# Performance work log

Measured on AMD Instinct MI355X. Metric: run time of the kernel, lower is better.

The kernel has to match this reference:

```python
import jax, jax.numpy as jnp
import numpy as np

IN_FEAT = 512   # input_feature_size
ACT_FEAT = 512  # action_feature_size
HIDDEN = 1024   # output_feature_size
L, B = 128, 64


def setup_inputs() -> dict:
    key = jax.random.key(0)
    ks = jax.random.split(key, 4)
    scale = 1.0 / np.sqrt(HIDDEN)
    return {
        "input_feature": jax.random.normal(ks[0], (B, IN_FEAT), jnp.float32),
        "action_features_data": jax.random.normal(ks[1], (L, B, ACT_FEAT), jnp.float32),
        "hidden_state": jnp.zeros((B, HIDDEN), jnp.float32),
        "state": jnp.zeros((B, HIDDEN), jnp.float32),
        "W_ih": jax.random.normal(ks[2], (4 * HIDDEN, IN_FEAT + ACT_FEAT), jnp.float32) * scale,
        "W_hh": jax.random.normal(ks[3], (4 * HIDDEN, HIDDEN), jnp.float32) * scale,
        "b_ih": jnp.zeros((4 * HIDDEN,), jnp.float32),
        "b_hh": jnp.zeros((4 * HIDDEN,), jnp.float32),
    }


def _lstm_forward(input_feature, acts, h0, c0, W_ih, W_hh, b_ih, b_hh):
    H = h0.shape[-1]
    # Split the input weight into the static (input_feature) and per-step (action) parts.
    W_x = W_ih[:, : input_feature.shape[-1]]   # [4H, in_feat]
    W_a = W_ih[:, input_feature.shape[-1]:]    # [4H, act_feat]
    # Precompute all input-side gate preactivations in one big GEMM: [L, B, 4H]
    pre = jnp.einsum("lba,ga->lbg", acts, W_a) + (input_feature @ W_x.T + b_ih + b_hh)

    def step(carry, pre_t):
        h, c = carry
        gates = pre_t + h @ W_hh.T            # [B, 4H]
        i, f, g, o = jnp.split(gates, 4, axis=-1)  # torch LSTMCell gate order
        i = jax.nn.sigmoid(i)
        f = jax.nn.sigmoid(f)
        g = jnp.tanh(g)
        o = jax.nn.sigmoid(o)
        c1 = f * c + i * g
        h1 = o * jnp.tanh(c1)
        return (h1, c1), h1

    (h_n, c_n), hs = jax.lax.scan(step, (h0, c0), pre)
    return hs, h_n, c_n


def reference(input_feature, action_features_data, hidden_state, state,
              W_ih, W_hh, b_ih, b_hh):
    return _lstm_forward(input_feature, action_features_data, hidden_state, state,
                         W_ih, W_hh, b_ih, b_hh)
```

## Files before the change

kernel.cpp:

```cpp
#include <hip/hip_runtime.h>
#include <hip/hip_bf16.h>

typedef __bf16 bf16x8 __attribute__((ext_vector_type(8)));
typedef float f32x4 __attribute__((ext_vector_type(4)));
typedef unsigned long long ull;

#define HN_OFF 8388608u
#define CN_OFF 8454144u

__device__ __forceinline__ float bf2f(ushort u) {
  union { unsigned int i; float f; } x; x.i = ((unsigned int)u) << 16; return x.f;
}
__device__ __forceinline__ ushort f2bf(float f) {
  union { float f; unsigned int i; } x; x.f = f;
  unsigned int r = x.i + 0x7FFFu + ((x.i >> 16) & 1u);
  return (ushort)(r >> 16);
}

__global__ __launch_bounds__(256) void conv_copy(const float* __restrict__ s,
                                                 ushort* __restrict__ d, int n4) {
  int i = blockIdx.x * 256 + threadIdx.x;
  if (i < n4) {
    float4 v = reinterpret_cast<const float4*>(s)[i];
    ushort4 o; o.x = f2bf(v.x); o.y = f2bf(v.y); o.z = f2bf(v.z); o.w = f2bf(v.w);
    reinterpret_cast<ushort4*>(d)[i] = o;
  }
}

__global__ __launch_bounds__(256) void conv_h0(const float* __restrict__ h0,
                                               ushort* __restrict__ hb) {
  int t = blockIdx.x * 256 + threadIdx.x;
  int b = t >> 7, c = t & 127;
  float4 v0 = *reinterpret_cast<const float4*>(h0 + (size_t)b * 1024 + c * 8);
  float4 v1 = *reinterpret_cast<const float4*>(h0 + (size_t)b * 1024 + c * 8 + 4);
  size_t de = ((size_t)(b >> 4) * 32 + (c >> 2)) * 512 + (size_t)(c & 3) * 128 + (b & 15) * 8;
  ushort* d = hb + de;
  d[0] = f2bf(v0.x); d[1] = f2bf(v0.y); d[2] = f2bf(v0.z); d[3] = f2bf(v0.w);
  d[4] = f2bf(v1.x); d[5] = f2bf(v1.y); d[6] = f2bf(v1.z); d[7] = f2bf(v1.w);
}

__global__ __launch_bounds__(256) void conv_wa(const float* __restrict__ Wih,
                                               ushort* __restrict__ Wa) {
  int t = blockIdx.x * 256 + threadIdx.x;
  int g = t >> 7, c = t & 127;
  float4 v = *reinterpret_cast<const float4*>(Wih + (size_t)g * 1024 + 512 + c * 4);
  ushort4 o; o.x = f2bf(v.x); o.y = f2bf(v.y); o.z = f2bf(v.z); o.w = f2bf(v.w);
  *reinterpret_cast<ushort4*>(Wa + (size_t)g * 512 + c * 4) = o;
}

__global__ __launch_bounds__(256) void base_kernel(const float* __restrict__ x,
    const float* __restrict__ Wih, const float* __restrict__ bih,
    const float* __restrict__ bhh, float* __restrict__ baseT) {
  int t = blockIdx.x * 256 + threadIdx.x;
  int g = t >> 6, b = t & 63;
  const float4* xv = reinterpret_cast<const float4*>(x + (size_t)b * 512);
  const float4* wv = reinterpret_cast<const float4*>(Wih + (size_t)g * 1024);
  float s = 0.f;
  #pragma unroll 4
  for (int a = 0; a < 128; ++a) {
    float4 xa = xv[a], wa = wv[a];
    s += xa.x * wa.x + xa.y * wa.y + xa.z * wa.z + xa.w * wa.w;
  }
  baseT[t] = s + bih[g] + bhh[g];
}

__global__ __launch_bounds__(256, 1) void gemm_pre(
    const ushort* __restrict__ A,
    const ushort* __restrict__ B,
    const float* __restrict__ baseT,
    ushort* __restrict__ C) {
  __shared__ ushort At[128 * 64];
  __shared__ ushort Bt[128 * 64];
  const int tid = threadIdx.x;
  const int m0 = blockIdx.x * 128;
  const int n0 = blockIdx.y * 128;
  const int wave = tid >> 6, lane = tid & 63;
  const int wm = wave >> 1, wn = wave & 1;
  const int q = lane >> 4, lc = lane & 15;

  f32x4 acc[4][4];
  #pragma unroll
  for (int mt = 0; mt < 4; ++mt)
    #pragma unroll
    for (int nt = 0; nt < 4; ++nt)
      acc[mt][nt] = (f32x4){0.f, 0.f, 0.f, 0.f};

  for (int k0 = 0; k0 < 512; k0 += 64) {
    __syncthreads();
    for (int idx = tid; idx < 1024; idx += 256) {
      int r = idx >> 3, ch = idx & 7;
      *reinterpret_cast<uint4*>(&At[r * 64 + (ch ^ (r & 7)) * 8]) =
          *reinterpret_cast<const uint4*>(A + (size_t)(m0 + r) * 512 + k0 + ch * 8);
      *reinterpret_cast<uint4*>(&Bt[r * 64 + (ch ^ (r & 7)) * 8]) =
          *reinterpret_cast<const uint4*>(B + (size_t)(n0 + r) * 512 + k0 + ch * 8);
    }
    __syncthreads();
    #pragma unroll
    for (int kk = 0; kk < 2; ++kk) {
      bf16x8 af[4], bfr[4];
      #pragma unroll
      for (int mt = 0; mt < 4; ++mt) {
        int r = wm * 64 + mt * 16 + lc;
        af[mt] = *reinterpret_cast<const bf16x8*>(&At[r * 64 + ((kk * 4 + q) ^ (r & 7)) * 8]);
      }
      #pragma unroll
      for (int nt = 0; nt < 4; ++nt) {
        int r = wn * 64 + nt * 16 + lc;
        bfr[nt] = *reinterpret_cast<const bf16x8*>(&Bt[r * 64 + ((kk * 4 + q) ^ (r & 7)) * 8]);
      }
      #pragma unroll
      for (int mt = 0; mt < 4; ++mt)
        #pragma unroll
        for (int nt = 0; nt < 4; ++nt)
          acc[mt][nt] = __builtin_amdgcn_mfma_f32_16x16x32_bf16(af[mt], bfr[nt], acc[mt][nt], 0, 0, 0);
    }
  }
  #pragma unroll
  for (int mt = 0; mt < 4; ++mt) {
    #pragma unroll
    for (int nt = 0; nt < 4; ++nt) {
      int g = m0 + wm * 64 + mt * 16 + q * 4;
      int lb = n0 + wn * 64 + nt * 16 + lc;
      int b = lb & 63;
      #pragma unroll
      for (int i = 0; i < 4; ++i) {
        float v = acc[mt][nt][i] + baseT[(size_t)(g + i) * 64 + b];
        C[(size_t)(g + i) * 8192 + lb] = f2bf(v);
      }
    }
  }
}

#define WAITG(n) asm volatile("s_waitcnt vmcnt(" #n ")" ::: "memory"); \
                 __builtin_amdgcn_sched_barrier(0);

__global__ __launch_bounds__(256, 1) void lstm_rec(
    const ushort* __restrict__ Whh,
    const ushort* __restrict__ pre,
    const float* __restrict__ c0,
    const ushort* __restrict__ hbuf,
    ushort* __restrict__ hbw,
    float* __restrict__ out,
    int* __restrict__ flags) {
  __shared__ ushort hl[32 * 512];
  __shared__ ushort hstage[16 * 16];
  const int tid = threadIdx.x;
  const int bid = blockIdx.x;
  const int bq = bid & 3;
  const int ug = bid >> 2;
  const int w = tid >> 6;
  const int lane = tid & 63;
  const int q = lane >> 4;
  const int lc = lane & 15;
  const int ul = w * 4 + (lc & 3);
  const int u = ug * 16 + ul;
  const int gr = u + ((lc >> 2) << 10);
  const int bbase = bq * 16 + q * 4;
  const bool cellLane = ((lc & 12) == 0);

  bf16x8 wfr[32];
  {
    const ushort* wr = Whh + (size_t)gr * 1024 + q * 8;
    #pragma unroll
    for (int kk = 0; kk < 32; ++kk)
      wfr[kk] = *reinterpret_cast<const bf16x8*>(wr + kk * 32);
  }

  float cst[4];
  #pragma unroll
  for (int i = 0; i < 4; ++i)
    cst[i] = cellLane ? c0[(size_t)(bbase + i) * 1024 + u] : 0.f;

  const unsigned va_base = ((unsigned)gr * 8192u + (unsigned)bbase) * 2u;
  const unsigned hob0 = ((unsigned)bq << 15) | ((unsigned)(w * 8) << 10) |
                        ((unsigned)lane << 4);
  const int myflag = (bq * 64 + w * 16 + (lane & 15)) * 4;

  ushort4 pa = *reinterpret_cast<const ushort4*>(pre + (size_t)gr * 8192 + bbase);

  for (int t = 0; t < 128; ++t) {
    if (t > 0) {
      for (;;) {
        int f = __hip_atomic_load(&flags[myflag], __ATOMIC_RELAXED,
                                  __HIP_MEMORY_SCOPE_AGENT);
        if (__all(f >= t)) break;
      }
    }

    const int tn = (t < 127) ? t + 1 : t;
    ushort4 npa;
    {
      unsigned va = va_base + (unsigned)tn * 128u;
      asm volatile("global_load_dwordx2 %0, %1, %2" : "=v"(npa) : "v"(va), "s"(pre));
    }

    const unsigned hob = hob0 | ((unsigned)(t & 1) << 17);
    bf16x8 haf[8];
    #pragma unroll
    for (int k = 0; k < 8; ++k) {
      unsigned voff = hob + ((unsigned)k << 10);
      asm volatile("global_load_dwordx4 %0, %1, %2 sc0 sc1"
                   : "=v"(haf[k]) : "v"(voff), "s"(hbuf));
    }
    WAITG(0)
    #pragma unroll
    for (int k = 0; k < 8; ++k)
      *reinterpret_cast<bf16x8*>(&hl[(w * 8 + k) * 512 + lane * 8]) = haf[k];
    __syncthreads();

    f32x4 acc_a, acc_b;
    acc_a[0] = bf2f(pa.x); acc_a[1] = bf2f(pa.y); acc_a[2] = bf2f(pa.z); acc_a[3] = bf2f(pa.w);
    acc_b = (f32x4){0.f, 0.f, 0.f, 0.f};

    #pragma unroll
    for (int kk = 0; kk < 16; ++kk) {
      bf16x8 af = *reinterpret_cast<const bf16x8*>(&hl[kk * 512 + lane * 8]);
      acc_a = __builtin_amdgcn_mfma_f32_16x16x32_bf16(af, wfr[kk], acc_a, 0, 0, 0);
    }
    #pragma unroll
    for (int kk = 16; kk < 32; ++kk) {
      bf16x8 af = *reinterpret_cast<const bf16x8*>(&hl[kk * 512 + lane * 8]);
      acc_b = __builtin_amdgcn_mfma_f32_16x16x32_bf16(af, wfr[kk], acc_b, 0, 0, 0);
    }
    f32x4 acc;
    #pragma unroll
    for (int i = 0; i < 4; ++i) acc[i] = acc_a[i] + acc_b[i];

    float fv[4], gv[4], ov[4];
    #pragma unroll
    for (int i = 0; i < 4; ++i) {
      fv[i] = __shfl_xor(acc[i], 4, 64);
      gv[i] = __shfl_xor(acc[i], 8, 64);
      ov[i] = __shfl_xor(acc[i], 12, 64);
    }
    float hv[4];
    if (cellLane) {
      #pragma unroll
      for (int i = 0; i < 4; ++i) {
        float ig = 1.f / (1.f + __expf(-acc[i]));
        float fg = 1.f / (1.f + __expf(-fv[i]));
        float gg = tanhf(gv[i]);
        float og = 1.f / (1.f + __expf(-ov[i]));
        float cn = fg * cst[i] + ig * gg;
        hv[i] = og * tanhf(cn);
        cst[i] = cn;
        hstage[(q * 4 + i) * 16 + ul] = f2bf(hv[i]);
      }
    }

    if (t == 127) {
      if (cellLane) {
        #pragma unroll
        for (int i = 0; i < 4; ++i) {
          int b = bbase + i;
          out[((size_t)t * 64 + b) * 1024 + u] = hv[i];
          out[HN_OFF + (size_t)b * 1024 + u] = hv[i];
          out[CN_OFF + (size_t)b * 1024 + u] = cst[i];
        }
      }
      break;
    }

    __syncthreads();

    if (tid < 32) {
      int bl = tid >> 1, ci = tid & 1;
      const ull* src = reinterpret_cast<const ull*>(&hstage[bl * 16 + ci * 8]);
      size_t de = ((size_t)((t + 1) & 1) << 16) + ((size_t)bq << 14) +
                  ((size_t)(ug >> 1) << 9) +
                  (size_t)(((ug * 2 + ci) & 3) * 16 + bl) * 8;
      ull* dst = reinterpret_cast<ull*>(hbw + de);
      __hip_atomic_store(dst, src[0], __ATOMIC_RELAXED, __HIP_MEMORY_SCOPE_AGENT);
      __hip_atomic_store(dst + 1, src[1], __ATOMIC_RELAXED, __HIP_MEMORY_SCOPE_AGENT);
    }
    if (w == 0) {
      asm volatile("s_waitcnt vmcnt(0)" ::: "memory");
      if (tid == 0)
        __hip_atomic_store(&flags[(bq * 64 + ug) * 4], t + 1, __ATOMIC_RELAXED,
                           __HIP_MEMORY_SCOPE_AGENT);
    }

    if (cellLane) {
      #pragma unroll
      for (int i = 0; i < 4; ++i)
        out[((size_t)t * 64 + bbase + i) * 1024 + u] = hv[i];
    }

    pa = npa;
  }
}

extern "C" void kernel_launch(void* const* d_in, const int* in_sizes, int n_in,
                              void* d_out, int out_size, void* d_ws, size_t ws_size,
                              hipStream_t stream) {
  const float* input = (const float*)d_in[0];
  const float* acts  = (const float*)d_in[1];
  const float* h0    = (const float*)d_in[2];
  const float* c0    = (const float*)d_in[3];
  const float* Wih   = (const float*)d_in[4];
  const float* Whh   = (const float*)d_in[5];
  const float* bih   = (const float*)d_in[6];
  const float* bhh   = (const float*)d_in[7];
  float* out = (float*)d_out;

  char* ws = (char*)d_ws;
  ushort* pre   = (ushort*)(ws);
  ushort* actsb = (ushort*)(ws + 67108864);
  ushort* Wab   = (ushort*)(ws + 75497472);
  ushort* Whhb  = (ushort*)(ws + 79691776);
  float*  baseT = (float*) (ws + 88080384);
  ushort* hbuf  = (ushort*)(ws + 89128960);
  int*    flags = (int*)   (ws + 89391104);

  hipMemsetAsync(flags, 0, 8192, stream);
  conv_copy<<<4096, 256, 0, stream>>>(acts, actsb, 1048576);
  conv_copy<<<4096, 256, 0, stream>>>(Whh, Whhb, 1048576);
  conv_h0<<<32, 256, 0, stream>>>(h0, hbuf);
  conv_wa<<<2048, 256, 0, stream>>>(Wih, Wab);
  base_kernel<<<1024, 256, 0, stream>>>(input, Wih, bih, bhh, baseT);
  gemm_pre<<<dim3(32, 64), 256, 0, stream>>>(Wab, actsb, baseT, pre);
  lstm_rec<<<256, 256, 0, stream>>>(Whhb, pre, c0, hbuf, hbuf, out, flags);
}
```

Baseline: 777.4 us.

## Fuse precompute GEMM and LSTM recurrence into one persistent mega-kernel with readiness flags

Merges the fp32-to-bf16 conversions, the input-projection GEMM and the recurrent LSTM loop into one launch. Extra blocks compute the pre-activation tiles and bump per-tile ready counters, and the recurrent blocks poll those counters so the GEMM overlaps with the time loop. The recurrent step now loads h straight from global memory into registers in double-buffered chunks instead of staging it through LDS with a barrier. h is written per lane and signalled through an LDS counter. This removes several launches and the intermediate conversion buffers. The risks are deadlock if the 256 recurrent blocks are not all co-resident alongside the GEMM blocks, and contention between the two kinds of block.

Result: slower. 1.325 ms (median of 2 runs) (+70.4%).

```diff
diff --git a/kernel.cpp b/kernel.cpp
--- a/kernel.cpp
+++ b/kernel.cpp
@@ -16,15 +16,8 @@
   unsigned int r = x.i + 0x7FFFu + ((x.i >> 16) & 1u);
   return (ushort)(r >> 16);
 }
-
-__global__ __launch_bounds__(256) void conv_copy(const float* __restrict__ s,
-                                                 ushort* __restrict__ d, int n4) {
-  int i = blockIdx.x * 256 + threadIdx.x;
-  if (i < n4) {
-    float4 v = reinterpret_cast<const float4*>(s)[i];
-    ushort4 o; o.x = f2bf(v.x); o.y = f2bf(v.y); o.z = f2bf(v.z); o.w = f2bf(v.w);
-    reinterpret_cast<ushort4*>(d)[i] = o;
-  }
+__device__ __forceinline__ unsigned pack2(float a, float b) {
+  return (unsigned)f2bf(a) | ((unsigned)f2bf(b) << 16);
 }
 
 __global__ __launch_bounds__(256) void conv_h0(const float* __restrict__ h0,
@@ -37,15 +30,6 @@
   ushort* d = hb + de;
   d[0] = f2bf(v0.x); d[1] = f2bf(v0.y); d[2] = f2bf(v0.z); d[3] = f2bf(v0.w);
   d[4] = f2bf(v1.x); d[5] = f2bf(v1.y); d[6] = f2bf(v1.z); d[7] = f2bf(v1.w);
-}
-
-__global__ __launch_bounds__(256) void conv_wa(const float* __restrict__ Wih,
-                                               ushort* __restrict__ Wa) {
-  int t = blockIdx.x * 256 + threadIdx.x;
-  int g = t >> 7, c = t & 127;
-  float4 v = *reinterpret_cast<const float4*>(Wih + (size_t)g * 1024 + 512 + c * 4);
-  ushort4 o; o.x = f2bf(v.x); o.y = f2bf(v.y); o.z = f2bf(v.z); o.w = f2bf(v.w);
-  *reinterpret_cast<ushort4*>(Wa + (size_t)g * 512 + c * 4) = o;
 }
 
 __global__ __launch_bounds__(256) void base_kernel(const float* __restrict__ x,
@@ -64,88 +48,103 @@
   baseT[t] = s + bih[g] + bhh[g];
 }
 
-__global__ __launch_bounds__(256, 1) void gemm_pre(
-    const ushort* __restrict__ A,
-    const ushort* __restrict__ B,
-    const float* __restrict__ baseT,
-    ushort* __restrict__ C) {
-  __shared__ ushort At[128 * 64];
-  __shared__ ushort Bt[128 * 64];
-  const int tid = threadIdx.x;
-  const int m0 = blockIdx.x * 128;
-  const int n0 = blockIdx.y * 128;
-  const int wave = tid >> 6, lane = tid & 63;
-  const int wm = wave >> 1, wn = wave & 1;
-  const int q = lane >> 4, lc = lane & 15;
-
-  f32x4 acc[4][4];
-  #pragma unroll
-  for (int mt = 0; mt < 4; ++mt)
-    #pragma unroll
-    for (int nt = 0; nt < 4; ++nt)
-      acc[mt][nt] = (f32x4){0.f, 0.f, 0.f, 0.f};
-
-  for (int k0 = 0; k0 < 512; k0 += 64) {
-    __syncthreads();
-    for (int idx = tid; idx < 1024; idx += 256) {
-      int r = idx >> 3, ch = idx & 7;
-      *reinterpret_cast<uint4*>(&At[r * 64 + (ch ^ (r & 7)) * 8]) =
-          *reinterpret_cast<const uint4*>(A + (size_t)(m0 + r) * 512 + k0 + ch * 8);
-      *reinterpret_cast<uint4*>(&Bt[r * 64 + (ch ^ (r & 7)) * 8]) =
-          *reinterpret_cast<const uint4*>(B + (size_t)(n0 + r) * 512 + k0 + ch * 8);
-    }
-    __syncthreads();
-    #pragma unroll
-    for (int kk = 0; kk < 2; ++kk) {
-      bf16x8 af[4], bfr[4];
-      #pragma unroll
-      for (int mt = 0; mt < 4; ++mt) {
-        int r = wm * 64 + mt * 16 + lc;
-        af[mt] = *reinterpret_cast<const bf16x8*>(&At[r * 64 + ((kk * 4 + q) ^ (r & 7)) * 8]);
-      }
-      #pragma unroll
-      for (int nt = 0; nt < 4; ++nt) {
-        int r = wn * 64 + nt * 16 + lc;
-        bfr[nt] = *reinterpret_cast<const bf16x8*>(&Bt[r * 64 + ((kk * 4 + q) ^ (r & 7)) * 8]);
-      }
-      #pragma unroll
-      for (int mt = 0; mt < 4; ++mt)
-        #pragma unroll
-        for (int nt = 0; nt < 4; ++nt)
-          acc[mt][nt] = __builtin_amdgcn_mfma_f32_16x16x32_bf16(af[mt], bfr[nt], acc[mt][nt], 0, 0, 0);
-    }
-  }
-  #pragma unroll
-  for (int mt = 0; mt < 4; ++mt) {
-    #pragma unroll
-    for (int nt = 0; nt < 4; ++nt) {
-      int g = m0 + wm * 64 + mt * 16 + q * 4;
-      int lb = n0 + wn * 64 + nt * 16 + lc;
-      int b = lb & 63;
-      #pragma unroll
-      for (int i = 0; i < 4; ++i) {
-        float v = acc[mt][nt][i] + baseT[(size_t)(g + i) * 64 + b];
-        C[(size_t)(g + i) * 8192 + lb] = f2bf(v);
-      }
-    }
-  }
-}
-
 #define WAITG(n) asm volatile("s_waitcnt vmcnt(" #n ")" ::: "memory"); \
                  __builtin_amdgcn_sched_barrier(0);
 
-__global__ __launch_bounds__(256, 1) void lstm_rec(
-    const ushort* __restrict__ Whh,
-    const ushort* __restrict__ pre,
+__global__ __launch_bounds__(256, 2) void mega_kernel(
+    const float* __restrict__ Whh,
+    const float* __restrict__ Wih,
+    const float* __restrict__ acts,
     const float* __restrict__ c0,
-    const ushort* __restrict__ hbuf,
-    ushort* __restrict__ hbw,
+    const float* __restrict__ baseT,
+    ushort* hbuf,
+    ushort* pre,
     float* __restrict__ out,
-    int* __restrict__ flags) {
-  __shared__ ushort hl[32 * 512];
-  __shared__ ushort hstage[16 * 16];
+    int* flags) {
+  __shared__ char smem[32768];
+  const int bid = blockIdx.x;
   const int tid = threadIdx.x;
-  const int bid = blockIdx.x;
+  int* pre_ready = flags + 1024;
+
+  if (bid >= 256) {
+    ushort* At = (ushort*)smem;
+    ushort* Bt = (ushort*)(smem + 16384);
+    const int gb = bid - 256;
+    const int m0 = (gb & 31) * 128;
+    const int ntile = gb >> 5;
+    const int n0 = ntile * 128;
+    const int wave = tid >> 6, lane = tid & 63;
+    const int wm = wave >> 1, wn = wave & 1;
+    const int q = lane >> 4, lc = lane & 15;
+
+    f32x4 acc[4][4];
+    #pragma unroll
+    for (int mt = 0; mt < 4; ++mt)
+      #pragma unroll
+      for (int nt = 0; nt < 4; ++nt)
+        acc[mt][nt] = (f32x4){0.f, 0.f, 0.f, 0.f};
+
+    for (int k0 = 0; k0 < 512; k0 += 64) {
+      __syncthreads();
+      for (int idx = tid; idx < 1024; idx += 256) {
+        int r = idx >> 3, ch = idx & 7;
+        const float* ap = Wih + (size_t)(m0 + r) * 1024 + 512 + k0 + ch * 8;
+        float4 ax = *(const float4*)ap; float4 ay = *(const float4*)(ap + 4);
+        uint4 av; av.x = pack2(ax.x, ax.y); av.y = pack2(ax.z, ax.w);
+        av.z = pack2(ay.x, ay.y); av.w = pack2(ay.z, ay.w);
+        *reinterpret_cast<uint4*>(&At[r * 64 + (ch ^ (r & 7)) * 8]) = av;
+        const float* bp = acts + (size_t)(n0 + r) * 512 + k0 + ch * 8;
+        float4 bx = *(const float4*)bp; float4 by = *(const float4*)(bp + 4);
+        uint4 bv; bv.x = pack2(bx.x, bx.y); bv.y = pack2(bx.z, bx.w);
+        bv.z = pack2(by.x, by.y); bv.w = pack2(by.z, by.w);
+        *reinterpret_cast<uint4*>(&Bt[r * 64 + (ch ^ (r & 7)) * 8]) = bv;
+      }
+      __syncthreads();
+      #pragma unroll
+      for (int kk = 0; kk < 2; ++kk) {
+        bf16x8 af[4], bfr[4];
+        #pragma unroll
+        for (int mt = 0; mt < 4; ++mt) {
+          int r = wm * 64 + mt * 16 + lc;
+          af[mt] = *reinterpret_cast<const bf16x8*>(&At[r * 64 + ((kk * 4 + q) ^ (r & 7)) * 8]);
+        }
+        #pragma unroll
+        for (int nt = 0; nt < 4; ++nt) {
+          int r = wn * 64 + nt * 16 + lc;
+          bfr[nt] = *reinterpret_cast<const bf16x8*>(&Bt[r * 64 + ((kk * 4 + q) ^ (r & 7)) * 8]);
+        }
+        #pragma unroll
+        for (int mt = 0; mt < 4; ++mt)
+          #pragma unroll
+          for (int nt = 0; nt < 4; ++nt)
+            acc[mt][nt] = __builtin_amdgcn_mfma_f32_16x16x32_bf16(af[mt], bfr[nt], acc[mt][nt], 0, 0, 0);
+      }
+    }
+    #pragma unroll
+    for (int mt = 0; mt < 4; ++mt) {
+      #pragma unroll
+      for (int nt = 0; nt < 4; ++nt) {
+        int g = m0 + wm * 64 + mt * 16 + q * 4;
+        int lb = n0 + wn * 64 + nt * 16 + lc;
+        unsigned l = (unsigned)(lb >> 6), b = (unsigned)(lb & 63);
+        #pragma unroll
+        for (int i = 0; i < 4; ++i) {
+          float v = acc[mt][nt][i] + baseT[(size_t)(g + i) * 64 + b];
+          unsigned data = f2bf(v);
+          unsigned voff = (l * 262144u + (unsigned)(g + i) * 64u + b) * 2u;
+          asm volatile("global_store_short %0, %1, %2 sc0 sc1"
+                       :: "v"(voff), "v"(data), "s"(pre) : "memory");
+        }
+      }
+    }
+    asm volatile("s_waitcnt vmcnt(0)" ::: "memory");
+    __syncthreads();
+    if (tid == 0)
+      __hip_atomic_fetch_add(&pre_ready[ntile], 1, __ATOMIC_RELAXED,
+                             __HIP_MEMORY_SCOPE_AGENT);
+    return;
+  }
+
   const int bq = bid & 3;
   const int ug = bid >> 2;
   const int w = tid >> 6;
@@ -158,70 +157,99 @@
   const int bbase = bq * 16 + q * 4;
   const bool cellLane = ((lc & 12) == 0);
 
+  int* cnt = (int*)smem;
+  if (tid == 0) { cnt[0] = 0; cnt[1] = 0; }
+
   bf16x8 wfr[32];
   {
-    const ushort* wr = Whh + (size_t)gr * 1024 + q * 8;
-    #pragma unroll
-    for (int kk = 0; kk < 32; ++kk)
-      wfr[kk] = *reinterpret_cast<const bf16x8*>(wr + kk * 32);
-  }
-
+    const float* wr = Whh + (size_t)gr * 1024 + q * 8;
+    #pragma unroll
+    for (int kk = 0; kk < 32; ++kk) {
+      float4 x = *(const float4*)(wr + kk * 32);
+      float4 y = *(const float4*)(wr + kk * 32 + 4);
+      uint4 p; p.x = pack2(x.x, x.y); p.y = pack2(x.z, x.w);
+      p.z = pack2(y.x, y.y); p.w = pack2(y.z, y.w);
+      wfr[kk] = *reinterpret_cast<bf16x8*>(&p);
+    }
+  }
   float cst[4];
   #pragma unroll
   for (int i = 0; i < 4; ++i)
     cst[i] = cellLane ? c0[(size_t)(bbase + i) * 1024 + u] : 0.f;
 
-  const unsigned va_base = ((unsigned)gr * 8192u + (unsigned)bbase) * 2u;
-  const unsigned hob0 = ((unsigned)bq << 15) | ((unsigned)(w * 8) << 10) |
-                        ((unsigned)lane << 4);
-  const int myflag = (bq * 64 + w * 16 + (lane & 15)) * 4;
-
-  ushort4 pa = *reinterpret_cast<const ushort4*>(pre + (size_t)gr * 8192 + bbase);
+  __syncthreads();
+
+  const unsigned hld = ((unsigned)bq << 15) | ((unsigned)lane << 4);
+  const unsigned hst = ((unsigned)((bq * 32 + (u >> 5)) * 512 +
+                                   ((u >> 3) & 3) * 128 + (q * 4) * 8 + (u & 7))) * 2u;
+  const unsigned pre_base = ((unsigned)(gr * 64 + bbase)) * 2u;
+  const int* fp = flags + bq * 64 + lane;
+  const int myflag = bq * 64 + ug;
+
+  for (;;) {
+    int r = __hip_atomic_load(&pre_ready[0], __ATOMIC_RELAXED, __HIP_MEMORY_SCOPE_AGENT);
+    if (__all(r >= 32)) break;
+    __builtin_amdgcn_s_sleep(2);
+  }
+  ushort4 pa = *reinterpret_cast<const ushort4*>(pre + (size_t)gr * 64 + bbase);
 
   for (int t = 0; t < 128; ++t) {
-    if (t > 0) {
-      for (;;) {
-        int f = __hip_atomic_load(&flags[myflag], __ATOMIC_RELAXED,
-                                  __HIP_MEMORY_SCOPE_AGENT);
-        if (__all(f >= t)) break;
-      }
-    }
-
     const int tn = (t < 127) ? t + 1 : t;
+    const int tile = tn >> 1;
+    for (;;) {
+      int f = (t > 0) ? __hip_atomic_load(fp, __ATOMIC_RELAXED, __HIP_MEMORY_SCOPE_AGENT)
+                      : 0x7fffffff;
+      int r = __hip_atomic_load(&pre_ready[tile], __ATOMIC_RELAXED, __HIP_MEMORY_SCOPE_AGENT);
+      if (__all((f >= t) && (r >= 32))) break;
+      __builtin_amdgcn_s_sleep(2);
+    }
+
     ushort4 npa;
-    {
-      unsigned va = va_base + (unsigned)tn * 128u;
-      asm volatile("global_load_dwordx2 %0, %1, %2" : "=v"(npa) : "v"(va), "s"(pre));
-    }
-
-    const unsigned hob = hob0 | ((unsigned)(t & 1) << 17);
-    bf16x8 haf[8];
-    #pragma unroll
-    for (int k = 0; k < 8; ++k) {
-      unsigned voff = hob + ((unsigned)k << 10);
+    asm volatile("global_load_dwordx2 %0, %1, %2 sc0 sc1"
+                 : "=v"(npa) : "v"(pre_base + (unsigned)tn * 524288u), "s"(pre));
+    const unsigned hob = hld | ((unsigned)(t & 1) << 17);
+    bf16x8 hA[8], hB[8];
+    #pragma unroll
+    for (int k = 0; k < 8; ++k)
       asm volatile("global_load_dwordx4 %0, %1, %2 sc0 sc1"
-                   : "=v"(haf[k]) : "v"(voff), "s"(hbuf));
-    }
+                   : "=v"(hA[k]) : "v"(hob + ((unsigned)k << 10)), "s"(hbuf));
+    #pragma unroll
+    for (int k = 0; k < 8; ++k)
+      asm volatile("global_load_dwordx4 %0, %1, %2 sc0 sc1"
+                   : "=v"(hB[k]) : "v"(hob + ((unsigned)(k + 8) << 10)), "s"(hbuf));
+
+    f32x4 acc_a, acc_b;
+    acc_a[0] = bf2f(pa.x); acc_a[1] = bf2f(pa.y);
+    acc_a[2] = bf2f(pa.z); acc_a[3] = bf2f(pa.w);
+    acc_b = (f32x4){0.f, 0.f, 0.f, 0.f};
+
+    WAITG(8)
+    #pragma unroll
+    for (int j = 0; j < 8; ++j)
+      acc_a = __builtin_amdgcn_mfma_f32_16x16x32_bf16(hA[j], wfr[j], acc_a, 0, 0, 0);
+    __builtin_amdgcn_sched_barrier(0);
+    #pragma unroll
+    for (int k = 0; k < 8; ++k)
+      asm volatile("global_load_dwordx4 %0, %1, %2 sc0 sc1"
+                   : "=v"(hA[k]) : "v"(hob + ((unsigned)(k + 16) << 10)), "s"(hbuf));
+    WAITG(8)
+    #pragma unroll
+    for (int j = 0; j < 8; ++j)
+      acc_b = __builtin_amdgcn_mfma_f32_16x16x32_bf16(hB[j], wfr[8 + j], acc_b, 0, 0, 0);
+    __builtin_amdgcn_sched_barrier(0);
+    #pragma unroll
+    for (int k = 0; k < 8; ++k)
+      asm volatile("global_load_dwordx4 %0, %1, %2 sc0 sc1"
+                   : "=v"(hB[k]) : "v"(hob + ((unsigned)(k + 24) << 10)), "s"(hbuf));
+    WAITG(8)
+    #pragma unroll
+    for (int j = 0; j < 8; ++j)
+      acc_a = __builtin_amdgcn_mfma_f32_16x16x32_bf16(hA[j], wfr[16 + j], acc_a, 0, 0, 0);
     WAITG(0)
     #pragma unroll
-    for (int k = 0; k < 8; ++k)
-      *reinterpret_cast<bf16x8*>(&hl[(w * 8 + k) * 512 + lane * 8]) = haf[k];
-    __syncthreads();
-
-    f32x4 acc_a, acc_b;
-    acc_a[0] = bf2f(pa.x); acc_a[1] = bf2f(pa.y); acc_a[2] = bf2f(pa.z); acc_a[3] = bf2f(pa.w);
-    acc_b = (f32x4){0.f, 0.f, 0.f, 0.f};
-
-    #pragma unroll
-    for (int kk = 0; kk < 16; ++kk) {
-      bf16x8 af = *reinterpret_cast<const bf16x8*>(&hl[kk * 512 + lane * 8]);
-      acc_a = __builtin_amdgcn_mfma_f32_16x16x32_bf16(af, wfr[kk], acc_a, 0, 0, 0);
-    }
-    #pragma unroll
-    for (int kk = 16; kk < 32; ++kk) {
-      bf16x8 af = *reinterpret_cast<const bf16x8*>(&hl[kk * 512 + lane * 8]);
-      acc_b = __builtin_amdgcn_mfma_f32_16x16x32_bf16(af, wfr[kk], acc_b, 0, 0, 0);
-    }
+    for (int j = 0; j < 8; ++j)
+      acc_b = __builtin_amdgcn_mfma_f32_16x16x32_bf16(hB[j], wfr[24 + j], acc_b, 0, 0, 0);
+
     f32x4 acc;
     #pragma unroll
     for (int i = 0; i < 4; ++i) acc[i] = acc_a[i] + acc_b[i];
@@ -244,7 +272,6 @@
         float cn = fg * cst[i] + ig * gg;
         hv[i] = og * tanhf(cn);
         cst[i] = cn;
-        hstage[(q * 4 + i) * 16 + ul] = f2bf(hv[i]);
       }
     }
 
@@ -261,31 +288,29 @@
       break;
     }
 
-    __syncthreads();
-
-    if (tid < 32) {
-      int bl = tid >> 1, ci = tid & 1;
-      const ull* src = reinterpret_cast<const ull*>(&hstage[bl * 16 + ci * 8]);
-      size_t de = ((size_t)((t + 1) & 1) << 16) + ((size_t)bq << 14) +
-                  ((size_t)(ug >> 1) << 9) +
-                  (size_t)(((ug * 2 + ci) & 3) * 16 + bl) * 8;
-      ull* dst = reinterpret_cast<ull*>(hbw + de);
-      __hip_atomic_store(dst, src[0], __ATOMIC_RELAXED, __HIP_MEMORY_SCOPE_AGENT);
-      __hip_atomic_store(dst + 1, src[1], __ATOMIC_RELAXED, __HIP_MEMORY_SCOPE_AGENT);
-    }
-    if (w == 0) {
-      asm volatile("s_waitcnt vmcnt(0)" ::: "memory");
-      if (tid == 0)
-        __hip_atomic_store(&flags[(bq * 64 + ug) * 4], t + 1, __ATOMIC_RELAXED,
+    if (cellLane) {
+      #pragma unroll
+      for (int i = 0; i < 4; ++i) {
+        unsigned dv = f2bf(hv[i]);
+        unsigned voff = hst + (unsigned)(i * 16) + ((unsigned)((t + 1) & 1) << 17);
+        asm volatile("global_store_short %0, %1, %2 sc0 sc1"
+                     :: "v"(voff), "v"(dv), "s"(hbuf) : "memory");
+      }
+    }
+    WAITG(0)
+    if (lane == 0) {
+      int old = atomicAdd(&cnt[t & 1], 1);
+      if (old == 3) {
+        cnt[t & 1] = 0;
+        __hip_atomic_store(&flags[myflag], t + 1, __ATOMIC_RELAXED,
                            __HIP_MEMORY_SCOPE_AGENT);
-    }
-
+      }
+    }
     if (cellLane) {
       #pragma unroll
       for (int i = 0; i < 4; ++i)
         out[((size_t)t * 64 + bbase + i) * 1024 + u] = hv[i];
     }
-
     pa = npa;
   }
 }
@@ -305,19 +330,12 @@
 
   char* ws = (char*)d_ws;
   ushort* pre   = (ushort*)(ws);
-  ushort* actsb = (ushort*)(ws + 67108864);
-  ushort* Wab   = (ushort*)(ws + 75497472);
-  ushort* Whhb  = (ushort*)(ws + 79691776);
-  float*  baseT = (float*) (ws + 88080384);
-  ushort* hbuf  = (ushort*)(ws + 89128960);
-  int*    flags = (int*)   (ws + 89391104);
+  ushort* hbuf  = (ushort*)(ws + 67108864);
+  int*    flags = (int*)   (ws + 67371008);
+  float*  baseT = (float*) (ws + 67379200);
 
   hipMemsetAsync(flags, 0, 8192, stream);
-  conv_copy<<<4096, 256, 0, stream>>>(acts, actsb, 1048576);
-  conv_copy<<<4096, 256, 0, stream>>>(Whh, Whhb, 1048576);
   conv_h0<<<32, 256, 0, stream>>>(h0, hbuf);
-  conv_wa<<<2048, 256, 0, stream>>>(Wih, Wab);
   base_kernel<<<1024, 256, 0, stream>>>(input, Wih, bih, bhh, baseT);
-  gemm_pre<<<dim3(32, 64), 256, 0, stream>>>(Wab, actsb, baseT, pre);
-  lstm_rec<<<256, 256, 0, stream>>>(Whhb, pre, c0, hbuf, hbuf, out, flags);
-}
+  mega_kernel<<<2304, 256, 0, stream>>>(Whh, Wih, acts, c0, baseT, hbuf, pre, out, flags);
+}
```

## Fuse bf16 conversions into GEMM/recurrence and split recurrence K across waves

Applied to the files above, without the earlier changes.

Removes the separate fp32-to-bf16 conversion kernels for actions, W_a and W_hh, converting on load inside gemm_pre and in the recurrent kernel prologue. The recurrent kernel is restructured so each wave multiplies its own K-slice of h (loaded directly into registers) against four gate tiles, then reduces partial sums through shared memory. This removes the LDS staging of the full h vector and overlaps the MFMAs with the second half of the h loads. In exchange gemm_pre now reads fp32 data, doubling its global traffic, and each step adds a shared-memory reduction.

Measured after the change: 789.4 us. Within noise of the previous version (+1.5%).

```diff
diff --git a/kernel.cpp b/kernel.cpp
--- a/kernel.cpp
+++ b/kernel.cpp
@@ -16,15 +16,8 @@
   unsigned int r = x.i + 0x7FFFu + ((x.i >> 16) & 1u);
   return (ushort)(r >> 16);
 }
-
-__global__ __launch_bounds__(256) void conv_copy(const float* __restrict__ s,
-                                                 ushort* __restrict__ d, int n4) {
-  int i = blockIdx.x * 256 + threadIdx.x;
-  if (i < n4) {
-    float4 v = reinterpret_cast<const float4*>(s)[i];
-    ushort4 o; o.x = f2bf(v.x); o.y = f2bf(v.y); o.z = f2bf(v.z); o.w = f2bf(v.w);
-    reinterpret_cast<ushort4*>(d)[i] = o;
-  }
+__device__ __forceinline__ unsigned pack2(float a, float b) {
+  return (unsigned)f2bf(a) | ((unsigned)f2bf(b) << 16);
 }
 
 __global__ __launch_bounds__(256) void conv_h0(const float* __restrict__ h0,
@@ -37,15 +30,6 @@
   ushort* d = hb + de;
   d[0] = f2bf(v0.x); d[1] = f2bf(v0.y); d[2] = f2bf(v0.z); d[3] = f2bf(v0.w);
   d[4] = f2bf(v1.x); d[5] = f2bf(v1.y); d[6] = f2bf(v1.z); d[7] = f2bf(v1.w);
-}
-
-__global__ __launch_bounds__(256) void conv_wa(const float* __restrict__ Wih,
-                                               ushort* __restrict__ Wa) {
-  int t = blockIdx.x * 256 + threadIdx.x;
-  int g = t >> 7, c = t & 127;
-  float4 v = *reinterpret_cast<const float4*>(Wih + (size_t)g * 1024 + 512 + c * 4);
-  ushort4 o; o.x = f2bf(v.x); o.y = f2bf(v.y); o.z = f2bf(v.z); o.w = f2bf(v.w);
-  *reinterpret_cast<ushort4*>(Wa + (size_t)g * 512 + c * 4) = o;
 }
 
 __global__ __launch_bounds__(256) void base_kernel(const float* __restrict__ x,
@@ -65,8 +49,8 @@
 }
 
 __global__ __launch_bounds__(256, 1) void gemm_pre(
-    const ushort* __restrict__ A,
-    const ushort* __restrict__ B,
+    const float* __restrict__ Wih,
+    const float* __restrict__ acts,
     const float* __restrict__ baseT,
     ushort* __restrict__ C) {
   __shared__ ushort At[128 * 64];
@@ -89,10 +73,16 @@
     __syncthreads();
     for (int idx = tid; idx < 1024; idx += 256) {
       int r = idx >> 3, ch = idx & 7;
-      *reinterpret_cast<uint4*>(&At[r * 64 + (ch ^ (r & 7)) * 8]) =
-          *reinterpret_cast<const uint4*>(A + (size_t)(m0 + r) * 512 + k0 + ch * 8);
-      *reinterpret_cast<uint4*>(&Bt[r * 64 + (ch ^ (r & 7)) * 8]) =
-          *reinterpret_cast<const uint4*>(B + (size_t)(n0 + r) * 512 + k0 + ch * 8);
+      const float* ap = Wih + (size_t)(m0 + r) * 1024 + 512 + k0 + ch * 8;
+      float4 ax = *(const float4*)ap; float4 ay = *(const float4*)(ap + 4);
+      uint4 av; av.x = pack2(ax.x, ax.y); av.y = pack2(ax.z, ax.w);
+      av.z = pack2(ay.x, ay.y); av.w = pack2(ay.z, ay.w);
+      *reinterpret_cast<uint4*>(&At[r * 64 + (ch ^ (r & 7)) * 8]) = av;
+      const float* bp = acts + (size_t)(n0 + r) * 512 + k0 + ch * 8;
+      float4 bx = *(const float4*)bp; float4 by = *(const float4*)(bp + 4);
+      uint4 bv; bv.x = pack2(bx.x, bx.y); bv.y = pack2(bx.z, bx.w);
+      bv.z = pack2(by.x, by.y); bv.w = pack2(by.z, by.w);
+      *reinterpret_cast<uint4*>(&Bt[r * 64 + (ch ^ (r & 7)) * 8]) = bv;
     }
     __syncthreads();
     #pragma unroll
@@ -135,14 +125,14 @@
                  __builtin_amdgcn_sched_barrier(0);
 
 __global__ __launch_bounds__(256, 1) void lstm_rec(
-    const ushort* __restrict__ Whh,
+    const float* __restrict__ Whh,
     const ushort* __restrict__ pre,
     const float* __restrict__ c0,
     const ushort* __restrict__ hbuf,
     ushort* __restrict__ hbw,
     float* __restrict__ out,
     int* __restrict__ flags) {
-  __shared__ ushort hl[32 * 512];
+  __shared__ f32x4 part[4][4][64];
   __shared__ ushort hstage[16 * 16];
   const int tid = threadIdx.x;
   const int bid = blockIdx.x;
@@ -158,12 +148,19 @@
   const int bbase = bq * 16 + q * 4;
   const bool cellLane = ((lc & 12) == 0);
 
-  bf16x8 wfr[32];
-  {
-    const ushort* wr = Whh + (size_t)gr * 1024 + q * 8;
-    #pragma unroll
-    for (int kk = 0; kk < 32; ++kk)
-      wfr[kk] = *reinterpret_cast<const bf16x8*>(wr + kk * 32);
+  bf16x8 wfr[4][8];
+  #pragma unroll
+  for (int T = 0; T < 4; ++T) {
+    const int grT = ug * 16 + T * 4 + (lc & 3) + ((lc >> 2) << 10);
+    #pragma unroll
+    for (int k = 0; k < 8; ++k) {
+      const float* wp = Whh + (size_t)grT * 1024 + (w * 8 + k) * 32 + q * 8;
+      float4 x = *(const float4*)wp;
+      float4 y = *(const float4*)(wp + 4);
+      uint4 p; p.x = pack2(x.x, x.y); p.y = pack2(x.z, x.w);
+      p.z = pack2(y.x, y.y); p.w = pack2(y.z, y.w);
+      wfr[T][k] = *reinterpret_cast<bf16x8*>(&p);
+    }
   }
 
   float cst[4];
@@ -172,59 +169,60 @@
     cst[i] = cellLane ? c0[(size_t)(bbase + i) * 1024 + u] : 0.f;
 
   const unsigned va_base = ((unsigned)gr * 8192u + (unsigned)bbase) * 2u;
-  const unsigned hob0 = ((unsigned)bq << 15) | ((unsigned)(w * 8) << 10) |
-                        ((unsigned)lane << 4);
-  const int myflag = (bq * 64 + w * 16 + (lane & 15)) * 4;
+  const unsigned hob0 = ((unsigned)bq << 15) | ((unsigned)lane << 4);
+  const int* fp = flags + (bq * 64 + lane) * 4;
+  const int myflag = (bq * 64 + ug) * 4;
 
   ushort4 pa = *reinterpret_cast<const ushort4*>(pre + (size_t)gr * 8192 + bbase);
 
   for (int t = 0; t < 128; ++t) {
     if (t > 0) {
       for (;;) {
-        int f = __hip_atomic_load(&flags[myflag], __ATOMIC_RELAXED,
-                                  __HIP_MEMORY_SCOPE_AGENT);
+        int f = __hip_atomic_load(fp, __ATOMIC_RELAXED, __HIP_MEMORY_SCOPE_AGENT);
         if (__all(f >= t)) break;
       }
     }
 
     const int tn = (t < 127) ? t + 1 : t;
     ushort4 npa;
-    {
-      unsigned va = va_base + (unsigned)tn * 128u;
-      asm volatile("global_load_dwordx2 %0, %1, %2" : "=v"(npa) : "v"(va), "s"(pre));
-    }
-
+    asm volatile("global_load_dwordx2 %0, %1, %2"
+                 : "=v"(npa) : "v"(va_base + (unsigned)tn * 128u), "s"(pre));
     const unsigned hob = hob0 | ((unsigned)(t & 1) << 17);
     bf16x8 haf[8];
     #pragma unroll
-    for (int k = 0; k < 8; ++k) {
-      unsigned voff = hob + ((unsigned)k << 10);
+    for (int k = 0; k < 8; ++k)
       asm volatile("global_load_dwordx4 %0, %1, %2 sc0 sc1"
-                   : "=v"(haf[k]) : "v"(voff), "s"(hbuf));
+                   : "=v"(haf[k]) : "v"(hob + ((unsigned)(w * 8 + k) << 10)), "s"(hbuf));
+
+    f32x4 p0 = (f32x4){0.f,0.f,0.f,0.f}, p1 = p0, p2 = p0, p3 = p0;
+    WAITG(4)
+    #pragma unroll
+    for (int k = 0; k < 4; ++k) {
+      p0 = __builtin_amdgcn_mfma_f32_16x16x32_bf16(haf[k], wfr[0][k], p0, 0, 0, 0);
+      p1 = __builtin_amdgcn_mfma_f32_16x16x32_bf16(haf[k], wfr[1][k], p1, 0, 0, 0);
+      p2 = __builtin_amdgcn_mfma_f32_16x16x32_bf16(haf[k], wfr[2][k], p2, 0, 0, 0);
+      p3 = __builtin_amdgcn_mfma_f32_16x16x32_bf16(haf[k], wfr[3][k], p3, 0, 0, 0);
     }
     WAITG(0)
     #pragma unroll
-    for (int k = 0; k < 8; ++k)
-      *reinterpret_cast<bf16x8*>(&hl[(w * 8 + k) * 512 + lane * 8]) = haf[k];
+    for (int k = 4; k < 8; ++k) {
+      p0 = __builtin_amdgcn_mfma_f32_16x16x32_bf16(haf[k], wfr[0][k], p0, 0, 0, 0);
+      p1 = __builtin_amdgcn_mfma_f32_16x16x32_bf16(haf[k], wfr[1][k], p1, 0, 0, 0);
+      p2 = __builtin_amdgcn_mfma_f32_16x16x32_bf16(haf[k], wfr[2][k], p2, 0, 0, 0);
+      p3 = __builtin_amdgcn_mfma_f32_16x16x32_bf16(haf[k], wfr[3][k], p3, 0, 0, 0);
+    }
+    part[w][0][lane] = p0; part[w][1][lane] = p1;
+    part[w][2][lane] = p2; part[w][3][lane] = p3;
     __syncthreads();
 
-    f32x4 acc_a, acc_b;
-    acc_a[0] = bf2f(pa.x); acc_a[1] = bf2f(pa.y); acc_a[2] = bf2f(pa.z); acc_a[3] = bf2f(pa.w);
-    acc_b = (f32x4){0.f, 0.f, 0.f, 0.f};
-
-    #pragma unroll
-    for (int kk = 0; kk < 16; ++kk) {
-      bf16x8 af = *reinterpret_cast<const bf16x8*>(&hl[kk * 512 + lane * 8]);
-      acc_a = __builtin_amdgcn_mfma_f32_16x16x32_bf16(af, wfr[kk], acc_a, 0, 0, 0);
-    }
-    #pragma unroll
-    for (int kk = 16; kk < 32; ++kk) {
-      bf16x8 af = *reinterpret_cast<const bf16x8*>(&hl[kk * 512 + lane * 8]);
-      acc_b = __builtin_amdgcn_mfma_f32_16x16x32_bf16(af, wfr[kk], acc_b, 0, 0, 0);
-    }
     f32x4 acc;
-    #pragma unroll
-    for (int i = 0; i < 4; ++i) acc[i] = acc_a[i] + acc_b[i];
+    acc[0] = bf2f(pa.x); acc[1] = bf2f(pa.y); acc[2] = bf2f(pa.z); acc[3] = bf2f(pa.w);
+    #pragma unroll
+    for (int wp = 0; wp < 4; ++wp) {
+      f32x4 pr = part[wp][w][lane];
+      #pragma unroll
+      for (int i = 0; i < 4; ++i) acc[i] += pr[i];
+    }
 
     float fv[4], gv[4], ov[4];
     #pragma unroll
@@ -276,7 +274,7 @@
     if (w == 0) {
       asm volatile("s_waitcnt vmcnt(0)" ::: "memory");
       if (tid == 0)
-        __hip_atomic_store(&flags[(bq * 64 + ug) * 4], t + 1, __ATOMIC_RELAXED,
+        __hip_atomic_store(&flags[myflag], t + 1, __ATOMIC_RELAXED,
                            __HIP_MEMORY_SCOPE_AGENT);
     }
 
@@ -305,19 +303,13 @@
 
   char* ws = (char*)d_ws;
   ushort* pre   = (ushort*)(ws);
-  ushort* actsb = (ushort*)(ws + 67108864);
-  ushort* Wab   = (ushort*)(ws + 75497472);
-  ushort* Whhb  = (ushort*)(ws + 79691776);
-  float*  baseT = (float*) (ws + 88080384);
-  ushort* hbuf  = (ushort*)(ws + 89128960);
-  int*    flags = (int*)   (ws + 89391104);
+  ushort* hbuf  = (ushort*)(ws + 67108864);
+  int*    flags = (int*)   (ws + 67371008);
+  float*  baseT = (float*) (ws + 67379200);
 
   hipMemsetAsync(flags, 0, 8192, stream);
-  conv_copy<<<4096, 256, 0, stream>>>(acts, actsb, 1048576);
-  conv_copy<<<4096, 256, 0, stream>>>(Whh, Whhb, 1048576);
   conv_h0<<<32, 256, 0, stream>>>(h0, hbuf);
-  conv_wa<<<2048, 256, 0, stream>>>(Wih, Wab);
   base_kernel<<<1024, 256, 0, stream>>>(input, Wih, bih, bhh, baseT);
-  gemm_pre<<<dim3(32, 64), 256, 0, stream>>>(Wab, actsb, baseT, pre);
-  lstm_rec<<<256, 256, 0, stream>>>(Whhb, pre, c0, hbuf, hbuf, out, flags);
-}
+  gemm_pre<<<dim3(32, 64), 256, 0, stream>>>(Wih, acts, baseT, pre);
+  lstm_rec<<<256, 256, 0, stream>>>(Whh, pre, c0, hbuf, hbuf, out, flags);
+}
```
